# Kernel tuning notes

Hardware: AMD Instinct MI355X
Metric: run time of the kernel (lower is better)

## Reference

```python
import jax, jax.numpy as jnp
import numpy as np

N_NODES = 50000
N_EDGES = 800000
IN_CH = 128
HEADS = 4
HID = 32  # per-head dim; heads*hid = 128
N_GRAPHS = 128


def setup_inputs() -> dict:
    key = jax.random.key(0)
    ks = jax.random.split(key, 32)
    d = {}
    d["x"] = jax.random.normal(ks[0], (N_NODES, IN_CH), dtype=jnp.float32)
    d["edge_index"] = jax.random.randint(ks[1], (2, N_EDGES), 0, N_NODES, dtype=jnp.int64)
    d["batch"] = jnp.sort(jax.random.randint(ks[2], (N_NODES,), 0, N_GRAPHS, dtype=jnp.int64))
    HD = HEADS * HID
    names = [("wq1", (IN_CH, HD)), ("bq1", (HD,)), ("wk1", (IN_CH, HD)), ("bk1", (HD,)),
             ("wv1", (IN_CH, HD)), ("bv1", (HD,)), ("ws1", (IN_CH, HD)), ("bs1", (HD,)),
             ("wq2", (HD, HD)), ("bq2", (HD,)), ("wk2", (HD, HD)), ("bk2", (HD,)),
             ("wv2", (HD, HD)), ("bv2", (HD,)), ("ws2", (HD, HD)), ("bs2", (HD,)),
             ("wl", (HD, HD)), ("bl", (HD,)), ("wl2", (HD, 1)), ("bl2", (1,))]
    for i, (nm, shp) in enumerate(names):
        d[nm] = jax.random.normal(ks[3 + i], shp, dtype=jnp.float32) * 0.05
    return d


def _transformer_conv(x, src, dst, wq, bq, wk, bk, wv, bv, ws, bs):
    """PyG TransformerConv: multi-head dot-product attention over edges,
    softmax normalized per destination node, plus linear root/skip term."""
    N = x.shape[0]
    q = (x @ wq + bq).reshape(N, HEADS, HID)
    k = (x @ wk + bk).reshape(N, HEADS, HID)
    v = (x @ wv + bv).reshape(N, HEADS, HID)
    # edge scores: [E, H]
    e = jnp.einsum('ehd,ehd->eh', q[dst], k[src]) * np.float32(1.0 / np.sqrt(HID))
    # segment softmax over incoming edges of each destination node
    m = jax.ops.segment_max(e, dst, num_segments=N)
    a = jnp.exp(e - m[dst])
    s = jax.ops.segment_sum(a, dst, num_segments=N)
    alpha = a / s[dst]  # [E, H]
    msg = alpha[:, :, None] * v[src]  # [E, H, D]
    out = jax.ops.segment_sum(msg, dst, num_segments=N).reshape(N, HEADS * HID)
    return out + x @ ws + bs  # root weight (skip) term


def reference(x, edge_index, batch,
              wq1, bq1, wk1, bk1, wv1, bv1, ws1, bs1,
              wq2, bq2, wk2, bk2, wv2, bv2, ws2, bs2,
              wl, bl, wl2, bl2):
    src, dst = edge_index[0], edge_index[1]
    h = _transformer_conv(x, src, dst, wq1, bq1, wk1, bk1, wv1, bv1, ws1, bs1)
    h = jax.nn.relu(h)
    h = _transformer_conv(h, src, dst, wq2, bq2, wk2, bk2, wv2, bv2, ws2, bs2)
    h = jax.nn.relu(h)
    h = h @ wl + bl
    h = h @ wl2 + bl2  # [N, 1]
    # global mean pool over graphs
    sums = jax.ops.segment_sum(h, batch, num_segments=N_GRAPHS)
    cnts = jax.ops.segment_sum(jnp.ones((h.shape[0], 1), h.dtype), batch, num_segments=N_GRAPHS)
    return sums / jnp.maximum(cnts, 1.0)
```

## Files before the change

### kernel.cpp

```cpp
#include <hip/hip_runtime.h>
#include <hip/hip_bf16.h>
#include <math.h>

#define NNODES 50000
#define NEDGES 800000
#define NGRAPHS 128
#define SCAN_B ((NNODES + 255) / 256)

typedef __attribute__((ext_vector_type(8))) short bf16x8;
typedef __attribute__((ext_vector_type(4))) float f32x4;

__device__ __forceinline__ unsigned short f2bf(float f) {
    unsigned int u = __float_as_uint(f);
    return (unsigned short)((u + 0x7FFFu + ((u >> 16) & 1u)) >> 16);
}
__device__ __forceinline__ unsigned pack2bf(float a, float b) {
    return (unsigned)f2bf(a) | ((unsigned)f2bf(b) << 16);
}
__device__ __forceinline__ float2 bf2f2(unsigned int u) {
    float2 f;
    f.x = __uint_as_float(u << 16);
    f.y = __uint_as_float(u & 0xFFFF0000u);
    return f;
}

__global__ void count_edges(const int* __restrict__ ei, int* __restrict__ cnt) {
    int e = blockIdx.x * 256 + threadIdx.x;
    if (e < NEDGES) atomicAdd(&cnt[ei[NEDGES + e]], 1);
}

__global__ __launch_bounds__(256)
void scan_pass1(const int* __restrict__ cnt, int* __restrict__ bsum) {
    const int t = threadIdx.x;
    const int i = blockIdx.x * 256 + t;
    int v = (i < NNODES) ? cnt[i] : 0;
#pragma unroll
    for (int off = 32; off > 0; off >>= 1) v += __shfl_xor(v, off, 64);
    __shared__ int ws[4];
    if ((t & 63) == 0) ws[t >> 6] = v;
    __syncthreads();
    if (t == 0) bsum[blockIdx.x] = ws[0] + ws[1] + ws[2] + ws[3];
}

__global__ __launch_bounds__(256)
void scan_pass2(const int* __restrict__ bsum, int* __restrict__ boff) {
    const int t = threadIdx.x;
    const int v = (t < SCAN_B) ? bsum[t] : 0;
    __shared__ int a[256];
    a[t] = v;
    __syncthreads();
    for (int off = 1; off < 256; off <<= 1) {
        const int u = (t >= off) ? a[t - off] : 0;
        __syncthreads();
        a[t] += u;
        __syncthreads();
    }
    if (t < SCAN_B) boff[t] = a[t] - v;
}

__global__ __launch_bounds__(256)
void scan_pass3(const int* __restrict__ cnt, const int* __restrict__ boff,
                int* __restrict__ rowptr, int* __restrict__ wpos) {
    const int t = threadIdx.x;
    const int i = blockIdx.x * 256 + t;
    const int v = (i < NNODES) ? cnt[i] : 0;
    __shared__ int a[256];
    a[t] = v;
    __syncthreads();
    for (int off = 1; off < 256; off <<= 1) {
        const int u = (t >= off) ? a[t - off] : 0;
        __syncthreads();
        a[t] += u;
        __syncthreads();
    }
    if (i < NNODES) {
        const int e = boff[blockIdx.x] + a[t] - v;
        rowptr[i] = e;
        wpos[i]   = e;
    }
    if (i == 0) rowptr[NNODES] = NEDGES;
}

__global__ void fill_csr(const int* __restrict__ ei, int* __restrict__ wpos,
                         int* __restrict__ colsrc) {
    int e = blockIdx.x * 256 + threadIdx.x;
    if (e < NEDGES) {
        int d = ei[NEDGES + e];
        int slot = atomicAdd(&wpos[d], 1);
        colsrc[slot] = ei[e];
    }
}

__global__ void fuse_wl(const float* __restrict__ wl, const float* __restrict__ bl,
                        const float* __restrict__ wl2, const float* __restrict__ bl2,
                        float* __restrict__ wf, float* __restrict__ bf) {
    int t = threadIdx.x;
    float s = 0.f;
    for (int j = 0; j < 128; ++j) s += wl[t * 128 + j] * wl2[j];
    wf[t] = s;
    if (t == 0) {
        float s2 = 0.f;
        for (int j = 0; j < 128; ++j) s2 += bl[j] * wl2[j];
        bf[0] = s2 + bl2[0];
    }
}

__global__ void prep_w(const float* __restrict__ wq1, const float* __restrict__ wk1,
                       const float* __restrict__ wv1, const float* __restrict__ ws1,
                       const float* __restrict__ wq2, const float* __restrict__ wk2,
                       const float* __restrict__ wv2, const float* __restrict__ ws2,
                       unsigned short* __restrict__ Wt) {
    const int layer = blockIdx.z;
    const int sel   = blockIdx.y;
    const float* W = layer == 0
        ? (sel == 0 ? wq1 : sel == 1 ? wk1 : sel == 2 ? wv1 : ws1)
        : (sel == 0 ? wq2 : sel == 1 ? wk2 : sel == 2 ? wv2 : ws2);
    const int idx = blockIdx.x * 256 + threadIdx.x;
    const int col = idx & 127;
    const int k   = idx >> 7;
    Wt[layer * 65536 + sel * 16384 + col * 128 + k] = f2bf(W[k * 128 + col]);
}

template <bool A_BF16>
__global__ __launch_bounds__(256)
void gemm_qkvs(const void* __restrict__ Fv, const unsigned short* __restrict__ Wt,
               const float* __restrict__ bq, const float* __restrict__ bk,
               const float* __restrict__ bv, const float* __restrict__ bsk,
               unsigned short* __restrict__ Qb, unsigned short* __restrict__ Kb,
               unsigned short* __restrict__ Vb, unsigned short* __restrict__ Hb) {
    __shared__ __align__(16) unsigned short As[128][136];
    __shared__ __align__(16) unsigned short Bt[2][64][136];
    const int t    = threadIdx.x;
    const int m0   = blockIdx.x * 128;
    const int lane = t & 63;
    const int w    = t >> 6;
    const int l15  = lane & 15;
    const int lg   = lane >> 4;

    {
        const int row = t >> 1;
        const int kh  = (t & 1) * 64;
        const int gr  = min(m0 + row, NNODES - 1);
        if constexpr (A_BF16) {
            const unsigned short* src = &((const unsigned short*)Fv)[(size_t)gr * 128 + kh];
#pragma unroll
            for (int p = 0; p < 8; ++p)
                *(uint4*)&As[row][kh + p * 8] = *(const uint4*)&src[p * 8];
        } else {
            const float* src = &((const float*)Fv)[(size_t)gr * 128 + kh];
#pragma unroll
            for (int p = 0; p < 16; ++p) {
                const float4 v = *(const float4*)&src[p * 4];
                ushort4 u;
                u.x = f2bf(v.x); u.y = f2bf(v.y); u.z = f2bf(v.z); u.w = f2bf(v.w);
                *(ushort4*)&As[row][kh + p * 4] = u;
            }
        }
    }

#define STAGE_B(BUF, SL)                                                       \
    {                                                                          \
        const int sel_ = (SL) >> 1, c0_ = ((SL) & 1) * 64;                     \
        const int col = t >> 2, kb = (t & 3) * 32;                             \
        const unsigned short* src = &Wt[sel_ * 16384 + (c0_ + col) * 128 + kb];\
        _Pragma("unroll")                                                      \
        for (int p = 0; p < 4; ++p)                                            \
            *(uint4*)&Bt[BUF][col][kb + p * 8] = *(const uint4*)&src[p * 8];   \
    }

    STAGE_B(0, 0)
    __syncthreads();

    for (int sl = 0; sl < 8; ++sl) {
        const int cur = sl & 1;
        if (sl < 7) STAGE_B(cur ^ 1, sl + 1)

        const int sel = sl >> 1;
        const int c0  = (sl & 1) * 64;
        const float* bias = sel == 0 ? bq : sel == 1 ? bk : sel == 2 ? bv : bsk;
        unsigned short* Ob = sel == 0 ? Qb : sel == 1 ? Kb : sel == 2 ? Vb : Hb;

        const float b0 = bias[c0 + l15];
        const float b1 = bias[c0 + 16 + l15];
        const float b2 = bias[c0 + 32 + l15];
        const float b3 = bias[c0 + 48 + l15];
        f32x4 a00 = {b0, b0, b0, b0}, a01 = {b1, b1, b1, b1},
              a02 = {b2, b2, b2, b2}, a03 = {b3, b3, b3, b3};
        f32x4 a10 = a00, a11 = a01, a12 = a02, a13 = a03;
#pragma unroll
        for (int ks = 0; ks < 4; ++ks) {
            const int kof = ks * 32 + lg * 8;
            const bf16x8 af0 = *(const bf16x8*)&As[w * 32 + l15][kof];
            const bf16x8 af1 = *(const bf16x8*)&As[w * 32 + 16 + l15][kof];
            const bf16x8 bf0 = *(const bf16x8*)&Bt[cur][l15][kof];
            const bf16x8 bf1 = *(const bf16x8*)&Bt[cur][16 + l15][kof];
            const bf16x8 bf2 = *(const bf16x8*)&Bt[cur][32 + l15][kof];
            const bf16x8 bf3 = *(const bf16x8*)&Bt[cur][48 + l15][kof];
            a00 = __builtin_amdgcn_mfma_f32_16x16x32_bf16(af0, bf0, a00, 0, 0, 0);
            a01 = __builtin_amdgcn_mfma_f32_16x16x32_bf16(af0, bf1, a01, 0, 0, 0);
            a02 = __builtin_amdgcn_mfma_f32_16x16x32_bf16(af0, bf2, a02, 0, 0, 0);
            a03 = __builtin_amdgcn_mfma_f32_16x16x32_bf16(af0, bf3, a03, 0, 0, 0);
            a10 = __builtin_amdgcn_mfma_f32_16x16x32_bf16(af1, bf0, a10, 0, 0, 0);
            a11 = __builtin_amdgcn_mfma_f32_16x16x32_bf16(af1, bf1, a11, 0, 0, 0);
            a12 = __builtin_amdgcn_mfma_f32_16x16x32_bf16(af1, bf2, a12, 0, 0, 0);
            a13 = __builtin_amdgcn_mfma_f32_16x16x32_bf16(af1, bf3, a13, 0, 0, 0);
        }

        const int r0 = m0 + w * 32 + lg * 4;
#define STB(ACC, RT, CT)                                                       \
        _Pragma("unroll")                                                      \
        for (int i = 0; i < 4; ++i) {                                          \
            const int gr = r0 + (RT) * 16 + i;                                 \
            if (gr < NNODES)                                                   \
                Ob[(size_t)gr * 128 + c0 + (CT) * 16 + l15] = f2bf(ACC[i]);    \
        }
        STB(a00, 0, 0) STB(a01, 0, 1) STB(a02, 0, 2) STB(a03, 0, 3)
        STB(a10, 1, 0) STB(a11, 1, 1) STB(a12, 1, 2) STB(a13, 1, 3)
#undef STB
        __syncthreads();
    }
#undef STAGE_B
}

template <bool FUSE_HEAD>
__global__ __launch_bounds__(128)
void attn_agg(const unsigned short* __restrict__ Qb,
              const unsigned short* __restrict__ Kb,
              const unsigned short* __restrict__ Vb,
              unsigned short* __restrict__ Hb,
              const int* __restrict__ rowptr, const int* __restrict__ colsrc,
              const float* __restrict__ wf, float* __restrict__ r) {
    const int n    = blockIdx.x * 2 + (threadIdx.x >> 6);
    const int l    = threadIdx.x & 63;
    const int half = l >> 5;
    const int c    = (l & 31) * 4;
    const uint2 qu = *(const uint2*)&Qb[(size_t)n * 128 + c];
    const float2 q01 = bf2f2(qu.x), q23 = bf2f2(qu.y);
    const float sc_ = 0.17677669529663687f;
    const float q0 = q01.x * sc_, q1 = q01.y * sc_;
    const float q2 = q23.x * sc_, q3 = q23.y * sc_;
    const int beg = rowptr[n], end = rowptr[n + 1];
    const int cnt = end - beg;

    float m = -INFINITY, s = 0.f;
    float a0 = 0.f, a1 = 0.f, a2 = 0.f, a3 = 0.f;

    uint2 ku, vu;
    if (cnt > 0) {
        const int src = colsrc[min(beg + half, end - 1)];
        ku = *(const uint2*)&Kb[(size_t)src * 128 + c];
        vu = *(const uint2*)&Vb[(size_t)src * 128 + c];
    }
    for (int i = beg; i < end; i += 2) {
        const uint2 kc = ku, vc = vu;
        const bool valid = (i + half) < end;
        if (i + 2 < end) {
            const int srcN = colsrc[min(i + 2 + half, end - 1)];
            ku = *(const uint2*)&Kb[(size_t)srcN * 128 + c];
            vu = *(const uint2*)&Vb[(size_t)srcN * 128 + c];
        }
        const float2 k01 = bf2f2(kc.x), k23 = bf2f2(kc.y);
        float p = fmaf(q0, k01.x, fmaf(q1, k01.y, fmaf(q2, k23.x, q3 * k23.y)));
        p += __shfl_xor(p, 4);
        p += __shfl_xor(p, 2);
        p += __shfl_xor(p, 1);
        if (!valid) p = -INFINITY;
        const float pO = __shfl_xor(p, 32);
        const float nm = fmaxf(fmaxf(p, pO), m);
        const float sc = __expf(m - nm);
        const float w  = __expf(p - nm);
        s = fmaf(s, sc, w);
        const float2 v01 = bf2f2(vc.x), v23 = bf2f2(vc.y);
        a0 = fmaf(a0, sc, w * v01.x);
        a1 = fmaf(a1, sc, w * v01.y);
        a2 = fmaf(a2, sc, w * v23.x);
        a3 = fmaf(a3, sc, w * v23.y);
        m = nm;
    }
    s  += __shfl_xor(s, 32);
    a0 += __shfl_xor(a0, 32);
    a1 += __shfl_xor(a1, 32);
    a2 += __shfl_xor(a2, 32);
    a3 += __shfl_xor(a3, 32);

    const uint2 hu = *(const uint2*)&Hb[(size_t)n * 128 + c];
    const float2 h01 = bf2f2(hu.x), h23 = bf2f2(hu.y);
    float o0 = h01.x, o1 = h01.y, o2 = h23.x, o3 = h23.y;
    if (cnt > 0) {
        const float inv = 1.f / s;
        o0 = fmaf(a0, inv, o0);
        o1 = fmaf(a1, inv, o1);
        o2 = fmaf(a2, inv, o2);
        o3 = fmaf(a3, inv, o3);
    }
    o0 = fmaxf(o0, 0.f); o1 = fmaxf(o1, 0.f);
    o2 = fmaxf(o2, 0.f); o3 = fmaxf(o3, 0.f);
    if (!FUSE_HEAD) {
        if (half == 0) {
            uint2 o;
            o.x = pack2bf(o0, o1);
            o.y = pack2bf(o2, o3);
            *(uint2*)&Hb[(size_t)n * 128 + c] = o;
        }
    } else {
        const float4 w4 = *(const float4*)&wf[c];
        float val = fmaf(o0, w4.x, fmaf(o1, w4.y, fmaf(o2, w4.z, o3 * w4.w)));
        val += __shfl_xor(val, 16);
        val += __shfl_xor(val, 8);
        val += __shfl_xor(val, 4);
        val += __shfl_xor(val, 2);
        val += __shfl_xor(val, 1);
        if (l == 0) r[n] = val;
    }
}

__global__ __launch_bounds__(256)
void graph_pool(const float* __restrict__ r, const int* __restrict__ batch,
                const float* __restrict__ bf, float* __restrict__ out) {
    const int g = blockIdx.x;
    const int t = threadIdx.x;
    int lo = 0, hi = NNODES;
    while (lo < hi) { int mid = (lo + hi) >> 1; if (batch[mid] < g) lo = mid + 1; else hi = mid; }
    const int beg = lo;
    lo = beg; hi = NNODES;
    while (lo < hi) { int mid = (lo + hi) >> 1; if (batch[mid] < g + 1) lo = mid + 1; else hi = mid; }
    const int end = lo;

    float s = 0.f;
    for (int i = beg + t; i < end; i += 256) s += r[i];
#pragma unroll
    for (int off = 32; off > 0; off >>= 1) s += __shfl_xor(s, off, 64);
    __shared__ float pw[4];
    if ((t & 63) == 0) pw[t >> 6] = s;
    __syncthreads();
    if (t == 0) {
        const float cnt = (float)(end - beg);
        const float tot = pw[0] + pw[1] + pw[2] + pw[3] + cnt * bf[0];
        out[g] = tot / fmaxf(cnt, 1.f);
    }
}

extern "C" void kernel_launch(void* const* d_in, const int* in_sizes, int n_in,
                              void* d_out, int out_size, void* d_ws, size_t ws_size,
                              hipStream_t stream) {
    const float* x     = (const float*)d_in[0];
    const int*   ei    = (const int*)d_in[1];
    const int*   batch = (const int*)d_in[2];
    const float* wq1 = (const float*)d_in[3];  const float* bq1 = (const float*)d_in[4];
    const float* wk1 = (const float*)d_in[5];  const float* bk1 = (const float*)d_in[6];
    const float* wv1 = (const float*)d_in[7];  const float* bv1 = (const float*)d_in[8];
    const float* ws1 = (const float*)d_in[9];  const float* bs1 = (const float*)d_in[10];
    const float* wq2 = (const float*)d_in[11]; const float* bq2 = (const float*)d_in[12];
    const float* wk2 = (const float*)d_in[13]; const float* bk2 = (const float*)d_in[14];
    const float* wv2 = (const float*)d_in[15]; const float* bv2 = (const float*)d_in[16];
    const float* ws2 = (const float*)d_in[17]; const float* bs2 = (const float*)d_in[18];
    const float* wl  = (const float*)d_in[19]; const float* bl  = (const float*)d_in[20];
    const float* wl2 = (const float*)d_in[21]; const float* bl2 = (const float*)d_in[22];

    char* wsb = (char*)d_ws;
    size_t off = 0;
    auto carve = [&](size_t bytes) -> void* {
        void* p = wsb + off;
        off = (off + bytes + 255) & ~(size_t)255;
        return p;
    };
    const size_t NB = (size_t)NNODES * 128 * 2;
    unsigned short* Qb = (unsigned short*)carve(NB);
    unsigned short* Kb = (unsigned short*)carve(NB);
    unsigned short* Vb = (unsigned short*)carve(NB);
    unsigned short* H1 = (unsigned short*)carve(NB);
    unsigned short* H2 = (unsigned short*)carve(NB);
    int*   rowptr = (int*)carve((NNODES + 1) * sizeof(int));
    int*   wpos   = (int*)carve(NNODES * sizeof(int));
    int*   cnt    = (int*)carve(NNODES * sizeof(int));
    int*   colsrc = (int*)carve(NEDGES * sizeof(int));
    int*   bsum   = (int*)carve(256 * sizeof(int));
    int*   boff   = (int*)carve(256 * sizeof(int));
    float* wf     = (float*)carve(129 * sizeof(float));
    float* bf     = wf + 128;
    float* nodeval = (float*)carve(NNODES * sizeof(float));
    unsigned short* Wt = (unsigned short*)carve(131072 * sizeof(unsigned short));

    hipMemsetAsync(cnt, 0, NNODES * sizeof(int), stream);

    count_edges<<<(NEDGES + 255) / 256, 256, 0, stream>>>(ei, cnt);
    scan_pass1<<<SCAN_B, 256, 0, stream>>>(cnt, bsum);
    scan_pass2<<<1, 256, 0, stream>>>(bsum, boff);
    scan_pass3<<<SCAN_B, 256, 0, stream>>>(cnt, boff, rowptr, wpos);
    fill_csr<<<(NEDGES + 255) / 256, 256, 0, stream>>>(ei, wpos, colsrc);
    fuse_wl<<<1, 128, 0, stream>>>(wl, bl, wl2, bl2, wf, bf);
    prep_w<<<dim3(64, 4, 2), 256, 0, stream>>>(wq1, wk1, wv1, ws1,
                                               wq2, wk2, wv2, ws2, Wt);

    const int ggrid = (NNODES + 127) / 128;
    const int agrid = NNODES / 2;
    gemm_qkvs<false><<<ggrid, 256, 0, stream>>>(x, Wt, bq1, bk1, bv1, bs1,
                                                Qb, Kb, Vb, H1);
    attn_agg<false><<<agrid, 128, 0, stream>>>(Qb, Kb, Vb, H1, rowptr, colsrc,
                                               nullptr, nullptr);
    gemm_qkvs<true><<<ggrid, 256, 0, stream>>>(H1, Wt + 65536, bq2, bk2, bv2, bs2,
                                               Qb, Kb, Vb, H2);
    attn_agg<true><<<agrid, 128, 0, stream>>>(Qb, Kb, Vb, H2, rowptr, colsrc,
                                              wf, nodeval);
    graph_pool<<<NGRAPHS, 256, 0, stream>>>(nodeval, batch, bf, (float*)d_out);
}
```

Before: 392.8 us.

## Process four edges per wavefront with 8-wide vector loads and lazy softmax rescale

The attention aggregation now splits each 64-lane wavefront into four groups of 16 lanes, each lane handling 8 channels with 16-byte loads, so four edges are processed per iteration instead of two. The online softmax switches to exp2 with pre-scaled queries and rescales the running max only when a score exceeds it by more than a threshold, which removes per-edge exponentials and rescale multiplies. The fuse_wl prologue kernel is spread across 129 blocks with wavefront reductions instead of one serial block. This costs more registers per lane and extra cross-group shuffles at the end, and the lazy rescale allows accumulated weights to grow up to 2^8 before renormalising.

```diff
diff --git a/kernel.cpp b/kernel.cpp
--- a/kernel.cpp
+++ b/kernel.cpp
@@ -91,17 +91,19 @@
     }
 }
 
-__global__ void fuse_wl(const float* __restrict__ wl, const float* __restrict__ bl,
-                        const float* __restrict__ wl2, const float* __restrict__ bl2,
-                        float* __restrict__ wf, float* __restrict__ bf) {
-    int t = threadIdx.x;
-    float s = 0.f;
-    for (int j = 0; j < 128; ++j) s += wl[t * 128 + j] * wl2[j];
-    wf[t] = s;
-    if (t == 0) {
-        float s2 = 0.f;
-        for (int j = 0; j < 128; ++j) s2 += bl[j] * wl2[j];
-        bf[0] = s2 + bl2[0];
+__global__ __launch_bounds__(64)
+void fuse_wl(const float* __restrict__ wl, const float* __restrict__ bl,
+             const float* __restrict__ wl2, const float* __restrict__ bl2,
+             float* __restrict__ wf, float* __restrict__ bf) {
+    const int g = blockIdx.x;
+    const int l = threadIdx.x;
+    const float* row = (g < 128) ? &wl[g * 128] : bl;
+    float s = row[l] * wl2[l] + row[64 + l] * wl2[64 + l];
+#pragma unroll
+    for (int off = 32; off > 0; off >>= 1) s += __shfl_xor(s, off, 64);
+    if (l == 0) {
+        if (g < 128) wf[g] = s;
+        else         bf[0] = s + bl2[0];
     }
 }
 
@@ -230,82 +232,102 @@
               unsigned short* __restrict__ Hb,
               const int* __restrict__ rowptr, const int* __restrict__ colsrc,
               const float* __restrict__ wf, float* __restrict__ r) {
-    const int n    = blockIdx.x * 2 + (threadIdx.x >> 6);
-    const int l    = threadIdx.x & 63;
-    const int half = l >> 5;
-    const int c    = (l & 31) * 4;
-    const uint2 qu = *(const uint2*)&Qb[(size_t)n * 128 + c];
-    const float2 q01 = bf2f2(qu.x), q23 = bf2f2(qu.y);
-    const float sc_ = 0.17677669529663687f;
-    const float q0 = q01.x * sc_, q1 = q01.y * sc_;
-    const float q2 = q23.x * sc_, q3 = q23.y * sc_;
+    const int n = blockIdx.x * 2 + (threadIdx.x >> 6);
+    const int l = threadIdx.x & 63;
+    const int e = l >> 4;
+    const int c = (l & 15) * 8;
+    const uint4 qu = *(const uint4*)&Qb[(size_t)n * 128 + c];
+    const float S = 0.17677669529663687f * 1.4426950408889634f;
+    const float2 t01 = bf2f2(qu.x), t23 = bf2f2(qu.y);
+    const float2 t45 = bf2f2(qu.z), t67 = bf2f2(qu.w);
+    const float q0 = t01.x * S, q1 = t01.y * S, q2 = t23.x * S, q3 = t23.y * S;
+    const float q4 = t45.x * S, q5 = t45.y * S, q6 = t67.x * S, q7 = t67.y * S;
     const int beg = rowptr[n], end = rowptr[n + 1];
     const int cnt = end - beg;
 
     float m = -INFINITY, s = 0.f;
     float a0 = 0.f, a1 = 0.f, a2 = 0.f, a3 = 0.f;
-
-    uint2 ku, vu;
+    float a4 = 0.f, a5 = 0.f, a6 = 0.f, a7 = 0.f;
+
+    uint4 ku, vu;
     if (cnt > 0) {
-        const int src = colsrc[min(beg + half, end - 1)];
-        ku = *(const uint2*)&Kb[(size_t)src * 128 + c];
-        vu = *(const uint2*)&Vb[(size_t)src * 128 + c];
-    }
-    for (int i = beg; i < end; i += 2) {
-        const uint2 kc = ku, vc = vu;
-        const bool valid = (i + half) < end;
-        if (i + 2 < end) {
-            const int srcN = colsrc[min(i + 2 + half, end - 1)];
-            ku = *(const uint2*)&Kb[(size_t)srcN * 128 + c];
-            vu = *(const uint2*)&Vb[(size_t)srcN * 128 + c];
+        const int src = colsrc[min(beg + e, end - 1)];
+        ku = *(const uint4*)&Kb[(size_t)src * 128 + c];
+        vu = *(const uint4*)&Vb[(size_t)src * 128 + c];
+    }
+    for (int i = beg; i < end; i += 4) {
+        const uint4 kc = ku, vc = vu;
+        const bool valid = (i + e) < end;
+        if (i + 4 < end) {
+            const int srcN = colsrc[min(i + 4 + e, end - 1)];
+            ku = *(const uint4*)&Kb[(size_t)srcN * 128 + c];
+            vu = *(const uint4*)&Vb[(size_t)srcN * 128 + c];
         }
         const float2 k01 = bf2f2(kc.x), k23 = bf2f2(kc.y);
-        float p = fmaf(q0, k01.x, fmaf(q1, k01.y, fmaf(q2, k23.x, q3 * k23.y)));
-        p += __shfl_xor(p, 4);
+        const float2 k45 = bf2f2(kc.z), k67 = bf2f2(kc.w);
+        float p = q0 * k01.x;
+        p = fmaf(q1, k01.y, p); p = fmaf(q2, k23.x, p); p = fmaf(q3, k23.y, p);
+        p = fmaf(q4, k45.x, p); p = fmaf(q5, k45.y, p); p = fmaf(q6, k67.x, p);
+        p = fmaf(q7, k67.y, p);
         p += __shfl_xor(p, 2);
         p += __shfl_xor(p, 1);
         if (!valid) p = -INFINITY;
-        const float pO = __shfl_xor(p, 32);
-        const float nm = fmaxf(fmaxf(p, pO), m);
-        const float sc = __expf(m - nm);
-        const float w  = __expf(p - nm);
-        s = fmaf(s, sc, w);
+        if (!__all(p <= m + 8.f)) {
+            float pm = fmaxf(p, __shfl_xor(p, 16));
+            pm = fmaxf(pm, __shfl_xor(pm, 32));
+            const float nm = fmaxf(m, pm);
+            const float sc = exp2f(m - nm);
+            s *= sc;
+            a0 *= sc; a1 *= sc; a2 *= sc; a3 *= sc;
+            a4 *= sc; a5 *= sc; a6 *= sc; a7 *= sc;
+            m = nm;
+        }
+        const float w = exp2f(p - m);
+        s += w;
         const float2 v01 = bf2f2(vc.x), v23 = bf2f2(vc.y);
-        a0 = fmaf(a0, sc, w * v01.x);
-        a1 = fmaf(a1, sc, w * v01.y);
-        a2 = fmaf(a2, sc, w * v23.x);
-        a3 = fmaf(a3, sc, w * v23.y);
-        m = nm;
-    }
-    s  += __shfl_xor(s, 32);
-    a0 += __shfl_xor(a0, 32);
-    a1 += __shfl_xor(a1, 32);
-    a2 += __shfl_xor(a2, 32);
-    a3 += __shfl_xor(a3, 32);
-
-    const uint2 hu = *(const uint2*)&Hb[(size_t)n * 128 + c];
+        const float2 v45 = bf2f2(vc.z), v67 = bf2f2(vc.w);
+        a0 = fmaf(w, v01.x, a0); a1 = fmaf(w, v01.y, a1);
+        a2 = fmaf(w, v23.x, a2); a3 = fmaf(w, v23.y, a3);
+        a4 = fmaf(w, v45.x, a4); a5 = fmaf(w, v45.y, a5);
+        a6 = fmaf(w, v67.x, a6); a7 = fmaf(w, v67.y, a7);
+    }
+    s  += __shfl_xor(s, 16);  s  += __shfl_xor(s, 32);
+    a0 += __shfl_xor(a0, 16); a0 += __shfl_xor(a0, 32);
+    a1 += __shfl_xor(a1, 16); a1 += __shfl_xor(a1, 32);
+    a2 += __shfl_xor(a2, 16); a2 += __shfl_xor(a2, 32);
+    a3 += __shfl_xor(a3, 16); a3 += __shfl_xor(a3, 32);
+    a4 += __shfl_xor(a4, 16); a4 += __shfl_xor(a4, 32);
+    a5 += __shfl_xor(a5, 16); a5 += __shfl_xor(a5, 32);
+    a6 += __shfl_xor(a6, 16); a6 += __shfl_xor(a6, 32);
+    a7 += __shfl_xor(a7, 16); a7 += __shfl_xor(a7, 32);
+
+    const uint4 hu = *(const uint4*)&Hb[(size_t)n * 128 + c];
     const float2 h01 = bf2f2(hu.x), h23 = bf2f2(hu.y);
+    const float2 h45 = bf2f2(hu.z), h67 = bf2f2(hu.w);
     float o0 = h01.x, o1 = h01.y, o2 = h23.x, o3 = h23.y;
+    float o4 = h45.x, o5 = h45.y, o6 = h67.x, o7 = h67.y;
     if (cnt > 0) {
         const float inv = 1.f / s;
-        o0 = fmaf(a0, inv, o0);
-        o1 = fmaf(a1, inv, o1);
-        o2 = fmaf(a2, inv, o2);
-        o3 = fmaf(a3, inv, o3);
-    }
-    o0 = fmaxf(o0, 0.f); o1 = fmaxf(o1, 0.f);
-    o2 = fmaxf(o2, 0.f); o3 = fmaxf(o3, 0.f);
+        o0 = fmaf(a0, inv, o0); o1 = fmaf(a1, inv, o1);
+        o2 = fmaf(a2, inv, o2); o3 = fmaf(a3, inv, o3);
+        o4 = fmaf(a4, inv, o4); o5 = fmaf(a5, inv, o5);
+        o6 = fmaf(a6, inv, o6); o7 = fmaf(a7, inv, o7);
+    }
+    o0 = fmaxf(o0, 0.f); o1 = fmaxf(o1, 0.f); o2 = fmaxf(o2, 0.f);
+    o3 = fmaxf(o3, 0.f); o4 = fmaxf(o4, 0.f); o5 = fmaxf(o5, 0.f);
+    o6 = fmaxf(o6, 0.f); o7 = fmaxf(o7, 0.f);
     if (!FUSE_HEAD) {
-        if (half == 0) {
-            uint2 o;
-            o.x = pack2bf(o0, o1);
-            o.y = pack2bf(o2, o3);
-            *(uint2*)&Hb[(size_t)n * 128 + c] = o;
+        if (e == 0) {
+            uint4 o;
+            o.x = pack2bf(o0, o1); o.y = pack2bf(o2, o3);
+            o.z = pack2bf(o4, o5); o.w = pack2bf(o6, o7);
+            *(uint4*)&Hb[(size_t)n * 128 + c] = o;
         }
     } else {
-        const float4 w4 = *(const float4*)&wf[c];
-        float val = fmaf(o0, w4.x, fmaf(o1, w4.y, fmaf(o2, w4.z, o3 * w4.w)));
-        val += __shfl_xor(val, 16);
+        const float4 wA = *(const float4*)&wf[c];
+        const float4 wB = *(const float4*)&wf[c + 4];
+        float val = fmaf(o0, wA.x, fmaf(o1, wA.y, fmaf(o2, wA.z, o3 * wA.w)));
+        val = fmaf(o4, wB.x, fmaf(o5, wB.y, fmaf(o6, wB.z, fmaf(o7, wB.w, val))));
         val += __shfl_xor(val, 8);
         val += __shfl_xor(val, 4);
         val += __shfl_xor(val, 2);
@@ -388,7 +410,7 @@
     scan_pass2<<<1, 256, 0, stream>>>(bsum, boff);
     scan_pass3<<<SCAN_B, 256, 0, stream>>>(cnt, boff, rowptr, wpos);
     fill_csr<<<(NEDGES + 255) / 256, 256, 0, stream>>>(ei, wpos, colsrc);
-    fuse_wl<<<1, 128, 0, stream>>>(wl, bl, wl2, bl2, wf, bf);
+    fuse_wl<<<129, 64, 0, stream>>>(wl, bl, wl2, bl2, wf, bf);
     prep_w<<<dim3(64, 4, 2), 256, 0, stream>>>(wq1, wk1, wv1, ws1,
                                                wq2, wk2, wv2, ws2, Wt);
 
```

Result: faster. 369.6 us (-5.9%).
